# Kernel tuning notes

Hardware: AMD Instinct MI355X
Metric: run time of the kernel (lower is better)

The kernel has to match this reference:

```python
import jax, jax.numpy as jnp
import numpy as np

B, T, D = 128, 197, 768          # batch, tokens, model dim
HEADS, HID_PER_HEAD = 12, 64
H = HEADS * HID_PER_HEAD         # lstm hidden size (== D by construction)


def _block_mask(in_per_head, hid_per_head, head_num):
    """Block-diagonal mask replicated over the 4 LSTM gates (i,f,g,o)."""
    Ht = hid_per_head * head_num
    Dt = in_per_head * head_num
    m = np.zeros((4 * Ht, Dt), np.float32)
    for h in range(head_num):
        for g in range(4):
            r0 = g * Ht + h * hid_per_head
            m[r0:r0 + hid_per_head, h * in_per_head:(h + 1) * in_per_head] = 1.0
    return jnp.asarray(m)


def setup_inputs() -> dict:
    key = jax.random.key(0)
    ks = jax.random.split(key, 16)
    s = 1.0 / np.sqrt(H)  # pytorch LSTM init scale
    u = lambda k, shape: jax.random.uniform(k, shape, jnp.float32, -s, s)
    mask_ih = _block_mask(D // HEADS, HID_PER_HEAD, HEADS)   # [4H, D]
    mask_hh = _block_mask(HID_PER_HEAD, HID_PER_HEAD, HEADS)  # [4H, H]
    inp = {
        "x": jax.random.normal(ks[0], (B, T, D), jnp.float32),
        "pre_w": u(ks[1], (D, D)),
        "pre_b": u(ks[2], (D,)),
        "w_ih_f": u(ks[3], (4 * H, D)) * mask_ih,
        "w_hh_f": u(ks[4], (4 * H, H)) * mask_hh,
        "b_ih_f": u(ks[5], (4 * H,)),
        "b_hh_f": u(ks[6], (4 * H,)),
        "w_ih_r": u(ks[7], (4 * H, D)) * mask_ih,
        "w_hh_r": u(ks[8], (4 * H, H)) * mask_hh,
        "b_ih_r": u(ks[9], (4 * H,)),
        "b_hh_r": u(ks[10], (4 * H,)),
        "proj_w": u(ks[11], (D, 2 * H)),
        "proj_b": u(ks[12], (D,)),
    }
    return inp


def _lstm_dir(x, w_ih, w_hh, b_ih, b_hh, reverse):
    # Precompute input contribution for all timesteps: [B,T,4H]
    xg = jnp.einsum('btd,gd->btg', x, w_ih) + b_ih + b_hh
    xs = jnp.swapaxes(xg, 0, 1)  # [T,B,4H]
    Bn = x.shape[0]

    def step(carry, gx):
        h, c = carry
        gates = gx + h @ w_hh.T
        i, f, g, o = jnp.split(gates, 4, axis=-1)  # pytorch gate order i,f,g,o
        i = jax.nn.sigmoid(i)
        f = jax.nn.sigmoid(f)
        g = jnp.tanh(g)
        o = jax.nn.sigmoid(o)
        c = f * c + i * g
        h = o * jnp.tanh(c)
        return (h, c), h

    init = (jnp.zeros((Bn, w_hh.shape[1]), x.dtype),
            jnp.zeros((Bn, w_hh.shape[1]), x.dtype))
    _, hs = jax.lax.scan(step, init, xs, reverse=reverse)  # outputs aligned to input order
    return jnp.swapaxes(hs, 0, 1)  # [B,T,H]


def reference(x, pre_w, pre_b, w_ih_f, w_hh_f, b_ih_f, b_hh_f,
              w_ih_r, w_hh_r, b_ih_r, b_hh_r, proj_w, proj_b):
    x = x @ pre_w.T + pre_b                      # pre_proj
    hf = _lstm_dir(x, w_ih_f, w_hh_f, b_ih_f, b_hh_f, reverse=False)
    hr = _lstm_dir(x, w_ih_r, w_hh_r, b_ih_r, b_hh_r, reverse=True)
    lstm_out = jnp.concatenate([hf, hr], axis=-1)  # [B,T,2H]
    return lstm_out @ proj_w.T + proj_b            # proj -> [B,T,D]
```

## Files before the change

kernel.cpp:

```cpp
#include <hip/hip_runtime.h>
#include <stdint.h>

#define DEV __device__ __forceinline__

typedef __attribute__((ext_vector_type(8))) short short8;
typedef __attribute__((ext_vector_type(4))) float floatx4;

#define BATCH 128
#define TT    197
#define DD    768
#define NH    12
#define NROWS (BATCH*TT)
#define G4H   3072

DEV uint16_t f2bf(float f) {
    union { float f; uint32_t u; } v; v.f = f;
    uint32_t r = (v.u + 0x7FFF + ((v.u >> 16) & 1)) >> 16;
    return (uint16_t)r;
}

DEV floatx4 mfma16(short8 a, short8 b, floatx4 c) {
    return __builtin_amdgcn_mfma_f32_16x16x32_bf16(a, b, c, 0, 0, 0);
}

DEV float sigf(float x)   { return __builtin_amdgcn_rcpf(1.0f + __expf(-x)); }
DEV float tanhf_(float x) { return 1.0f - 2.0f * __builtin_amdgcn_rcpf(1.0f + __expf(2.0f * x)); }

__global__ void cvt_bf16(const float* __restrict__ src, uint16_t* __restrict__ dst, int n4) {
    int i = blockIdx.x * blockDim.x + threadIdx.x;
    int stride = gridDim.x * blockDim.x;
    for (; i < n4; i += stride) {
        float4 v = ((const float4*)src)[i];
        ushort4 o;
        o.x = f2bf(v.x); o.y = f2bf(v.y); o.z = f2bf(v.z); o.w = f2bf(v.w);
        ((ushort4*)dst)[i] = o;
    }
}

template<int STORE_BF16, int REMAP>
__global__ __launch_bounds__(256) void gemm_bf16(
    const uint16_t* __restrict__ A,
    const uint16_t* __restrict__ Bw,
    const float*    __restrict__ bias,
    void*           __restrict__ C,
    int K, int Ntot)
{
    __shared__ __attribute__((aligned(16))) uint16_t Atile[8 * 512];
    __shared__ __attribute__((aligned(16))) uint16_t Btile[4 * 512];

    const int tid  = threadIdx.x;
    const int wv   = tid >> 6;
    const int lane = tid & 63;
    const int ln   = lane & 15;
    const int kq   = lane >> 4;
    const int m0   = blockIdx.y * 128;
    const int n0   = blockIdx.x * 64;

    floatx4 acc[2][4];
#pragma unroll
    for (int a = 0; a < 2; a++)
#pragma unroll
        for (int b = 0; b < 4; b++) acc[a][b] = (floatx4){0.f, 0.f, 0.f, 0.f};

    const uint16_t* Arow0 = A  + (size_t)(m0 + (2*wv+0)*16 + ln) * K + kq*8;
    const uint16_t* Arow1 = A  + (size_t)(m0 + (2*wv+1)*16 + ln) * K + kq*8;
    const uint16_t* Brow  = Bw + (size_t)(n0 + wv*16      + ln) * K + kq*8;

    uint16_t* Adst0 = &Atile[(2*wv+0)*512 + lane*8];
    uint16_t* Adst1 = &Atile[(2*wv+1)*512 + lane*8];
    uint16_t* Bdst  = &Btile[ wv     *512 + lane*8];

    for (int k0 = 0; k0 < K; k0 += 32) {
        uint4 a0 = *(const uint4*)(Arow0 + k0);
        uint4 a1 = *(const uint4*)(Arow1 + k0);
        uint4 bb = *(const uint4*)(Brow  + k0);
        __syncthreads();
        *(uint4*)Adst0 = a0;
        *(uint4*)Adst1 = a1;
        *(uint4*)Bdst  = bb;
        __syncthreads();
        short8 af0 = *(const short8*)&Atile[(2*wv+0)*512 + lane*8];
        short8 af1 = *(const short8*)&Atile[(2*wv+1)*512 + lane*8];
        short8 bf[4];
#pragma unroll
        for (int nt = 0; nt < 4; nt++) bf[nt] = *(const short8*)&Btile[nt*512 + lane*8];
#pragma unroll
        for (int nt = 0; nt < 4; nt++) {
            acc[0][nt] = mfma16(af0, bf[nt], acc[0][nt]);
            acc[1][nt] = mfma16(af1, bf[nt], acc[1][nt]);
        }
    }

#pragma unroll
    for (int mt = 0; mt < 2; mt++)
#pragma unroll
        for (int nt = 0; nt < 4; nt++) {
            int n = n0 + nt*16 + ln;
            float bv = bias[n];
#pragma unroll
            for (int r = 0; r < 4; r++) {
                int m = m0 + (2*wv+mt)*16 + kq*4 + r;
                float val = acc[mt][nt][r] + bv;
                int row;
                if (REMAP) { int b = m / 197; int t = m - b*197; row = t*128 + b; }
                else       { row = m; }
                if (STORE_BF16) ((uint16_t*)C)[(size_t)row * Ntot + n] = f2bf(val);
                else            ((float*)C)[(size_t)row * Ntot + n]    = val;
            }
        }
}

__global__ __launch_bounds__(256) void lstm_fused(
    const uint16_t* __restrict__ pre,
    const uint16_t* __restrict__ wih_f, const uint16_t* __restrict__ whh_f,
    const uint16_t* __restrict__ wih_r, const uint16_t* __restrict__ whh_r,
    const float* __restrict__ bih_f, const float* __restrict__ bhh_f,
    const float* __restrict__ bih_r, const float* __restrict__ bhh_r,
    uint16_t* __restrict__ hout)
{
    __shared__ __attribute__((aligned(16))) uint16_t hbuf[16][72];

    const int tid  = threadIdx.x;
    const int wv   = tid >> 6;
    const int lane = tid & 63;
    const int ln   = lane & 15;
    const int q    = lane >> 4;
    const int b0   = blockIdx.x * 16;
    const int head = blockIdx.y;
    const int dir  = blockIdx.z;
    const int ub   = wv * 16;

    const uint16_t* wih = dir ? wih_r : wih_f;
    const uint16_t* whh = dir ? whh_r : whh_f;
    const float*    bih = dir ? bih_r : bih_f;
    const float*    bhh = dir ? bhh_r : bhh_f;

    short8 aih[4][2], ahh[4][2];
#pragma unroll
    for (int t = 0; t < 4; t++) {
        size_t row = (size_t)(t*768 + head*64 + ub + ln);
#pragma unroll
        for (int s = 0; s < 2; s++) {
            aih[t][s] = *(const short8*)(wih + row*768 + head*64 + s*32 + q*8);
            ahh[t][s] = *(const short8*)(whh + row*768 + head*64 + s*32 + q*8);
        }
    }
    float biasv[4][4];
#pragma unroll
    for (int t = 0; t < 4; t++)
#pragma unroll
        for (int r = 0; r < 4; r++) {
            int row = t*768 + head*64 + ub + q*4 + r;
            biasv[t][r] = bih[row] + bhh[row];
        }

    for (int i = tid; i < 16*72; i += 256) ((uint16_t*)hbuf)[i] = 0;
    float c[4] = {0.f, 0.f, 0.f, 0.f};
    __syncthreads();

    const uint16_t* xbase = pre + head*64 + q*8;
    int t_cur = dir ? (TT - 1) : 0;
    const int tstep = dir ? -1 : 1;
    size_t xo = (size_t)(t_cur*128 + b0 + ln) * 768;
    short8 xv0 = *(const short8*)(xbase + xo);
    short8 xv1 = *(const short8*)(xbase + xo + 32);

    for (int step = 0; step < TT; step++) {
        short8 cx0 = xv0, cx1 = xv1;
        int t_next = t_cur + tstep;
        if (step + 1 < TT) {
            size_t xo2 = (size_t)(t_next*128 + b0 + ln) * 768;
            xv0 = *(const short8*)(xbase + xo2);
            xv1 = *(const short8*)(xbase + xo2 + 32);
        }
        short8 hb0 = *(const short8*)&hbuf[ln][0*32 + q*8];
        short8 hb1 = *(const short8*)&hbuf[ln][1*32 + q*8];

        floatx4 acc[4];
#pragma unroll
        for (int t = 0; t < 4; t++)
            acc[t] = (floatx4){biasv[t][0], biasv[t][1], biasv[t][2], biasv[t][3]};
#pragma unroll
        for (int t = 0; t < 4; t++) {
            acc[t] = mfma16(aih[t][0], cx0, acc[t]);
            acc[t] = mfma16(ahh[t][0], hb0, acc[t]);
            acc[t] = mfma16(aih[t][1], cx1, acc[t]);
            acc[t] = mfma16(ahh[t][1], hb1, acc[t]);
        }

        union { uint16_t s[4]; uint2 v; } hp;
#pragma unroll
        for (int r = 0; r < 4; r++) {
            float ig = sigf(acc[0][r]);
            float fg = sigf(acc[1][r]);
            float gg = tanhf_(acc[2][r]);
            float og = sigf(acc[3][r]);
            c[r] = fg * c[r] + ig * gg;
            float hv = og * tanhf_(c[r]);
            hp.s[r] = f2bf(hv);
        }

        __syncthreads();
        *(uint2*)&hbuf[ln][ub + q*4] = hp.v;
        __syncthreads();

        {
            int bl = tid >> 4;
            int dw = tid & 15;
            uint2 v = *(const uint2*)&hbuf[bl][dw*4];
            size_t off = ((size_t)(b0 + bl)*TT + t_cur) * 1536 + dir*768 + head*64 + dw*4;
            *(uint2*)(hout + off) = v;
        }
        t_cur = t_next;
    }
}

extern "C" void kernel_launch(void* const* d_in, const int* in_sizes, int n_in,
                              void* d_out, int out_size, void* d_ws, size_t ws_size,
                              hipStream_t stream) {
    (void)in_sizes; (void)n_in; (void)out_size; (void)ws_size;
    const float* x     = (const float*)d_in[0];
    const float* pre_w = (const float*)d_in[1];
    const float* pre_b = (const float*)d_in[2];
    const float* wihf  = (const float*)d_in[3];
    const float* whhf  = (const float*)d_in[4];
    const float* bihf  = (const float*)d_in[5];
    const float* bhhf  = (const float*)d_in[6];
    const float* wihr  = (const float*)d_in[7];
    const float* whhr  = (const float*)d_in[8];
    const float* bihr  = (const float*)d_in[9];
    const float* bhhr  = (const float*)d_in[10];
    const float* projw = (const float*)d_in[11];
    const float* projb = (const float*)d_in[12];
    float* out = (float*)d_out;

    uint16_t* W = (uint16_t*)d_ws;
    uint16_t* xb     = W; W += (size_t)NROWS * DD;
    uint16_t* bwpre  = W; W += (size_t)DD * DD;
    uint16_t* bwihf  = W; W += (size_t)G4H * DD;
    uint16_t* bwhhf  = W; W += (size_t)G4H * DD;
    uint16_t* bwihr  = W; W += (size_t)G4H * DD;
    uint16_t* bwhhr  = W; W += (size_t)G4H * DD;
    uint16_t* bwproj = W; W += (size_t)DD * 2 * DD;
    uint16_t* preb   = W; W += (size_t)NROWS * DD;
    uint16_t* houtb  = W; W += (size_t)NROWS * 2 * DD;

    auto cvt = [&](const float* s, uint16_t* d, size_t n) {
        int n4 = (int)(n / 4);
        int blocks = (n4 + 255) / 256; if (blocks > 4096) blocks = 4096;
        hipLaunchKernelGGL(cvt_bf16, dim3(blocks), dim3(256), 0, stream, s, d, n4);
    };
    cvt(x,     xb,     (size_t)NROWS * DD);
    cvt(pre_w, bwpre,  (size_t)DD * DD);
    cvt(wihf,  bwihf,  (size_t)G4H * DD);
    cvt(whhf,  bwhhf,  (size_t)G4H * DD);
    cvt(wihr,  bwihr,  (size_t)G4H * DD);
    cvt(whhr,  bwhhr,  (size_t)G4H * DD);
    cvt(projw, bwproj, (size_t)DD * 2 * DD);

    hipLaunchKernelGGL((gemm_bf16<1, 1>), dim3(12, 197), dim3(256), 0, stream,
                       xb, bwpre, pre_b, (void*)preb, DD, DD);
    hipLaunchKernelGGL(lstm_fused, dim3(8, 12, 2), dim3(256), 0, stream,
                       preb, bwihf, bwhhf, bwihr, bwhhr,
                       bihf, bhhf, bihr, bhhr, houtb);
    hipLaunchKernelGGL((gemm_bf16<0, 0>), dim3(12, 197), dim3(256), 0, stream,
                       houtb, bwproj, projb, (void*)out, 2 * DD, DD);
}
```

Before: 577.3 us.

## Enlarge GEMM tiles to 128x128 and load tiles via async global-to-LDS copies

Both dense projections move from a 128x64 block tile to 128x128, with a 2x2 wave grid where each wave computes a 4x4 set of MFMA tiles. The intent is to raise operand reuse per LDS load and halve the number of blocks. Tiles are staged with global_load_lds, which copies straight into shared memory without passing through registers. Only the two GEMMs change, and the LSTM kernel, likely the dominant cost, is untouched. Still no double buffering, so each k step waits on its load between two barriers.

```diff
diff --git a/kernel.cpp b/kernel.cpp
--- a/kernel.cpp
+++ b/kernel.cpp
@@ -25,6 +25,13 @@
 
 DEV float sigf(float x)   { return __builtin_amdgcn_rcpf(1.0f + __expf(-x)); }
 DEV float tanhf_(float x) { return 1.0f - 2.0f * __builtin_amdgcn_rcpf(1.0f + __expf(2.0f * x)); }
+
+DEV void async16(const uint16_t* g, uint16_t* l) {
+    __builtin_amdgcn_global_load_lds(
+        (const __attribute__((address_space(1))) unsigned int*)g,
+        (__attribute__((address_space(3))) unsigned int*)l,
+        16, 0, 0);
+}
 
 __global__ void cvt_bf16(const float* __restrict__ src, uint16_t* __restrict__ dst, int n4) {
     int i = blockIdx.x * blockDim.x + threadIdx.x;
@@ -38,68 +45,72 @@
 }
 
 template<int STORE_BF16, int REMAP>
-__global__ __launch_bounds__(256) void gemm_bf16(
+__global__ __launch_bounds__(256) void gemm128(
     const uint16_t* __restrict__ A,
     const uint16_t* __restrict__ Bw,
     const float*    __restrict__ bias,
     void*           __restrict__ C,
     int K, int Ntot)
 {
-    __shared__ __attribute__((aligned(16))) uint16_t Atile[8 * 512];
-    __shared__ __attribute__((aligned(16))) uint16_t Btile[4 * 512];
+    __shared__ __attribute__((aligned(16))) uint16_t As[128 * 32];
+    __shared__ __attribute__((aligned(16))) uint16_t Bs[128 * 32];
 
     const int tid  = threadIdx.x;
     const int wv   = tid >> 6;
     const int lane = tid & 63;
     const int ln   = lane & 15;
-    const int kq   = lane >> 4;
+    const int q    = lane >> 4;
     const int m0   = blockIdx.y * 128;
-    const int n0   = blockIdx.x * 64;
-
-    floatx4 acc[2][4];
-#pragma unroll
-    for (int a = 0; a < 2; a++)
+    const int n0   = blockIdx.x * 128;
+    const int wm   = wv >> 1;
+    const int wn   = wv & 1;
+
+    floatx4 acc[4][4];
+#pragma unroll
+    for (int a = 0; a < 4; a++)
 #pragma unroll
         for (int b = 0; b < 4; b++) acc[a][b] = (floatx4){0.f, 0.f, 0.f, 0.f};
 
-    const uint16_t* Arow0 = A  + (size_t)(m0 + (2*wv+0)*16 + ln) * K + kq*8;
-    const uint16_t* Arow1 = A  + (size_t)(m0 + (2*wv+1)*16 + ln) * K + kq*8;
-    const uint16_t* Brow  = Bw + (size_t)(n0 + wv*16      + ln) * K + kq*8;
-
-    uint16_t* Adst0 = &Atile[(2*wv+0)*512 + lane*8];
-    uint16_t* Adst1 = &Atile[(2*wv+1)*512 + lane*8];
-    uint16_t* Bdst  = &Btile[ wv     *512 + lane*8];
+    const uint16_t* gA0 = A  + (size_t)(m0 + (2*wv+0)*16 + ln) * K + q*8;
+    const uint16_t* gA1 = A  + (size_t)(m0 + (2*wv+1)*16 + ln) * K + q*8;
+    const uint16_t* gB0 = Bw + (size_t)(n0 + (2*wv+0)*16 + ln) * K + q*8;
+    const uint16_t* gB1 = Bw + (size_t)(n0 + (2*wv+1)*16 + ln) * K + q*8;
+    uint16_t* lA0 = &As[(2*wv+0) * 512];
+    uint16_t* lA1 = &As[(2*wv+1) * 512];
+    uint16_t* lB0 = &Bs[(2*wv+0) * 512];
+    uint16_t* lB1 = &Bs[(2*wv+1) * 512];
 
     for (int k0 = 0; k0 < K; k0 += 32) {
-        uint4 a0 = *(const uint4*)(Arow0 + k0);
-        uint4 a1 = *(const uint4*)(Arow1 + k0);
-        uint4 bb = *(const uint4*)(Brow  + k0);
-        __syncthreads();
-        *(uint4*)Adst0 = a0;
-        *(uint4*)Adst1 = a1;
-        *(uint4*)Bdst  = bb;
-        __syncthreads();
-        short8 af0 = *(const short8*)&Atile[(2*wv+0)*512 + lane*8];
-        short8 af1 = *(const short8*)&Atile[(2*wv+1)*512 + lane*8];
-        short8 bf[4];
-#pragma unroll
-        for (int nt = 0; nt < 4; nt++) bf[nt] = *(const short8*)&Btile[nt*512 + lane*8];
+        __syncthreads();
+        async16(gA0 + k0, lA0);
+        async16(gA1 + k0, lA1);
+        async16(gB0 + k0, lB0);
+        async16(gB1 + k0, lB1);
+        __syncthreads();
+
+        short8 af[4], bf[4];
+#pragma unroll
+        for (int mt = 0; mt < 4; mt++)
+            af[mt] = *(const short8*)&As[(wm*4 + mt)*512 + lane*8];
+#pragma unroll
+        for (int nt = 0; nt < 4; nt++)
+            bf[nt] = *(const short8*)&Bs[(wn*4 + nt)*512 + lane*8];
+#pragma unroll
+        for (int mt = 0; mt < 4; mt++)
+#pragma unroll
+            for (int nt = 0; nt < 4; nt++)
+                acc[mt][nt] = mfma16(af[mt], bf[nt], acc[mt][nt]);
+    }
+
+#pragma unroll
+    for (int mt = 0; mt < 4; mt++)
 #pragma unroll
         for (int nt = 0; nt < 4; nt++) {
-            acc[0][nt] = mfma16(af0, bf[nt], acc[0][nt]);
-            acc[1][nt] = mfma16(af1, bf[nt], acc[1][nt]);
-        }
-    }
-
-#pragma unroll
-    for (int mt = 0; mt < 2; mt++)
-#pragma unroll
-        for (int nt = 0; nt < 4; nt++) {
-            int n = n0 + nt*16 + ln;
+            int n = n0 + (wn*4 + nt)*16 + ln;
             float bv = bias[n];
 #pragma unroll
             for (int r = 0; r < 4; r++) {
-                int m = m0 + (2*wv+mt)*16 + kq*4 + r;
+                int m = m0 + (wm*4 + mt)*16 + q*4 + r;
                 float val = acc[mt][nt][r] + bv;
                 int row;
                 if (REMAP) { int b = m / 197; int t = m - b*197; row = t*128 + b; }
@@ -258,11 +269,11 @@
     cvt(whhr,  bwhhr,  (size_t)G4H * DD);
     cvt(projw, bwproj, (size_t)DD * 2 * DD);
 
-    hipLaunchKernelGGL((gemm_bf16<1, 1>), dim3(12, 197), dim3(256), 0, stream,
+    hipLaunchKernelGGL((gemm128<1, 1>), dim3(6, 197), dim3(256), 0, stream,
                        xb, bwpre, pre_b, (void*)preb, DD, DD);
     hipLaunchKernelGGL(lstm_fused, dim3(8, 12, 2), dim3(256), 0, stream,
                        preb, bwihf, bwhhf, bwihr, bwhhr,
                        bihf, bhhf, bihr, bhhr, houtb);
-    hipLaunchKernelGGL((gemm_bf16<0, 0>), dim3(12, 197), dim3(256), 0, stream,
+    hipLaunchKernelGGL((gemm128<0, 0>), dim3(6, 197), dim3(256), 0, stream,
                        houtb, bwproj, projb, (void*)out, 2 * DD, DD);
 }
```

Result: faster. 511.8 us (-11.3%).
